# Kernel optimization log

Hardware: AMD Instinct MI355X
Metric: run time of the kernel (lower is better)

The kernel has to match this reference:

```python
import jax, jax.numpy as jnp
import numpy as np

B, N, C, H = 2, 2048, 1024, 16
D = C // H  # head_dim = 64


def setup_inputs() -> dict:
    key = jax.random.key(0)
    ks = jax.random.split(key, 10)
    s = 0.02
    return {
        "x": jax.random.normal(ks[0], (B, N, C), dtype=jnp.float32),
        "gauge_theta": jax.random.normal(ks[1], (C,), dtype=jnp.float32),
        "Wg": jax.random.normal(ks[2], (C, C), dtype=jnp.float32) * s,
        "bg": jnp.zeros((C,), dtype=jnp.float32),
        "Wqkv": jax.random.normal(ks[3], (3 * C, C), dtype=jnp.float32) * s,
        "bqkv": jnp.zeros((3 * C,), dtype=jnp.float32),
        "Wproj": jax.random.normal(ks[4], (C, C), dtype=jnp.float32) * s,
        "bproj": jnp.zeros((C,), dtype=jnp.float32),
    }


def reference(x, gauge_theta, Wg, bg, Wqkv, bqkv, Wproj, bproj):
    # gauge-equivariant mixing: x = x + 0.1 * (Linear(x) * theta)
    x_gauge = (jnp.einsum('bnc,oc->bno', x, Wg) + bg) * gauge_theta  # [B,N,C]
    xg = x + 0.1 * x_gauge
    # fused qkv projection -> [B,N,3,H,D] -> q,k,v [B,H,N,D]
    qkv = (jnp.einsum('bnc,oc->bno', xg, Wqkv) + bqkv).reshape(B, N, 3, H, D)
    qkv = jnp.transpose(qkv, (2, 0, 3, 1, 4))
    q, k, v = qkv[0], qkv[1], qkv[2]
    scale = 1.0 / jnp.sqrt(jnp.float32(D))
    attn = jnp.einsum('bhnd,bhmd->bhnm', q, k) * scale  # explicit [B,H,N,N]
    attn = jax.nn.softmax(attn, axis=-1)  # eval mode: no noise, no dropout
    out = jnp.einsum('bhnm,bhmd->bhnd', attn, v)  # [B,H,N,D]
    out = jnp.transpose(out, (0, 2, 1, 3)).reshape(B, N, C)
    return jnp.einsum('bnc,oc->bno', out, Wproj) + bproj
```

## Files before the change

### kernel.cpp

```cpp
#include <hip/hip_runtime.h>
#include <stdint.h>

typedef __bf16 bf16x8 __attribute__((ext_vector_type(8)));
typedef __bf16 bf16x2 __attribute__((ext_vector_type(2)));
typedef float  f32x4  __attribute__((ext_vector_type(4)));
typedef unsigned int u32x4 __attribute__((ext_vector_type(4)));
typedef unsigned short u16;

__device__ __forceinline__ u16 f2bf(float f) {
    return __builtin_bit_cast(u16, (__bf16)f);
}

__device__ __forceinline__ unsigned pk_bf16(float a, float b) {
    bf16x2 r; r[0] = (__bf16)a; r[1] = (__bf16)b;
    return __builtin_bit_cast(unsigned, r);
}

__device__ __forceinline__ bf16x8 ld_frag(const u16* p) {
    u32x4 u = *(const u32x4*)p;
    return __builtin_bit_cast(bf16x8, u);
}

__device__ __forceinline__ void gload16(const u16* g, u16* l) {
    __builtin_amdgcn_global_load_lds(
        (__attribute__((address_space(1))) void*)g,
        (__attribute__((address_space(3))) void*)l,
        16, 0, 0);
}

__device__ __forceinline__ int xcd_swz(int nwg) {
    int h = blockIdx.y * gridDim.x + blockIdx.x;
    return (h & 7) * (nwg >> 3) + (h >> 3);
}

#define ATT_CSC 0.18033688011112042f

__global__ __launch_bounds__(256) void cvt_all(
    const float* __restrict__ x, const float* __restrict__ wg,
    const float* __restrict__ wqkv, const float* __restrict__ wproj,
    u16* __restrict__ xo, u16* __restrict__ wgo,
    u16* __restrict__ wqkvo, u16* __restrict__ wprojo)
{
    int i = blockIdx.x * 256 + threadIdx.x;
    const float4* in; uint2* out; int off;
    if (i < 1048576)      { in = (const float4*)x;     out = (uint2*)xo;     off = i; }
    else if (i < 1310720) { in = (const float4*)wg;    out = (uint2*)wgo;    off = i - 1048576; }
    else if (i < 2097152) { in = (const float4*)wqkv;  out = (uint2*)wqkvo;  off = i - 1310720; }
    else                  { in = (const float4*)wproj; out = (uint2*)wprojo; off = i - 2097152; }
    float4 v = in[off];
    uint2 o; o.x = pk_bf16(v.x, v.y); o.y = pk_bf16(v.z, v.w);
    out[off] = o;
}

__global__ __launch_bounds__(512, 6) void gemm_bt(
    const u16* __restrict__ A,
    const u16* __restrict__ W,
    const float* __restrict__ bias,
    u16* __restrict__ qo, u16* __restrict__ ko, u16* __restrict__ vTo)
{
    __shared__ alignas(16) u16 As[128 * 64];
    __shared__ alignas(16) u16 Bs[128 * 64];
    const int tid  = threadIdx.x;
    const int wave = tid >> 6, lane = tid & 63;
    const int lquad = lane >> 4, lcol = lane & 15;
    const int wr = (wave >> 2) * 64, wc = (wave & 3) * 32;
    const int swzid = xcd_swz(768);
    const int rowb = (swzid & 31) * 128, colb = (swzid >> 5) * 128;
    const int srow8 = lane >> 3;
    const int swc = (((lane & 7) ^ srow8) * 8);
    const int rs0 = ((0 * 4 + lquad) ^ (lcol & 7)) * 8;
    const int rs1 = ((1 * 4 + lquad) ^ (lcol & 7)) * 8;

    const u16* gA = A + (size_t)(rowb + wave * 8 + srow8) * 1024 + swc;
    const u16* gB = W + (size_t)(colb + wave * 8 + srow8) * 1024 + swc;
    u16* dA = As + wave * 512;
    u16* dB = Bs + wave * 512;

    f32x4 zero4 = {0.f, 0.f, 0.f, 0.f};
    f32x4 acc[4][2];
#pragma unroll
    for (int i = 0; i < 4; i++)
#pragma unroll
        for (int j = 0; j < 2; j++) acc[i][j] = zero4;

    for (int k0 = 0; k0 < 1024; k0 += 64) {
        __syncthreads();
        gload16(gA + k0, dA);
        gload16(gA + (size_t)64 * 1024 + k0, dA + 64 * 64);
        gload16(gB + k0, dB);
        gload16(gB + (size_t)64 * 1024 + k0, dB + 64 * 64);
        __syncthreads();
#pragma unroll
        for (int db = 0; db < 2; db++) {
            const int rsw = db ? rs1 : rs0;
            bf16x8 af[4], bfr[2];
#pragma unroll
            for (int t = 0; t < 4; t++) af[t]  = ld_frag(As + (wr + t * 16 + lcol) * 64 + rsw);
#pragma unroll
            for (int t = 0; t < 2; t++) bfr[t] = ld_frag(Bs + (wc + t * 16 + lcol) * 64 + rsw);
#pragma unroll
            for (int i = 0; i < 4; i++)
#pragma unroll
                for (int j = 0; j < 2; j++)
                    acc[i][j] = __builtin_amdgcn_mfma_f32_16x16x32_bf16(af[i], bfr[j], acc[i][j], 0, 0, 0);
        }
    }

#pragma unroll
    for (int i = 0; i < 4; i++) {
#pragma unroll
        for (int j = 0; j < 2; j++) {
            int gcol = colb + wc + j * 16 + lcol;
            float bsv = bias[gcol];
            int grow0 = rowb + wr + i * 16 + lquad * 4;
            int three = gcol >> 10, rem = gcol & 1023;
            int h = rem >> 6, d = rem & 63;
            int b = grow0 >> 11, nn = grow0 & 2047;
            int bh = b * 16 + h;
            if (three == 2) {
                ushort4 o;
                o.x = f2bf(acc[i][j][0] + bsv);
                o.y = f2bf(acc[i][j][1] + bsv);
                o.z = f2bf(acc[i][j][2] + bsv);
                o.w = f2bf(acc[i][j][3] + bsv);
                *(ushort4*)(vTo + ((size_t)bh * 64 + d) * 2048 + nn) = o;
            } else if (three == 0) {
#pragma unroll
                for (int r = 0; r < 4; r++)
                    qo[((size_t)bh * 2048 + nn + r) * 64 + d] = f2bf((acc[i][j][r] + bsv) * ATT_CSC);
            } else {
#pragma unroll
                for (int r = 0; r < 4; r++)
                    ko[((size_t)bh * 2048 + nn + r) * 64 + d] = f2bf(acc[i][j][r] + bsv);
            }
        }
    }
}

__global__ __launch_bounds__(512, 4) void gemm64(
    int mode,
    const u16* __restrict__ A,
    const u16* __restrict__ W,
    const float* __restrict__ bias,
    const float* __restrict__ xres,
    const float* __restrict__ theta,
    u16* __restrict__ out_bf,
    float* __restrict__ out_f)
{
    __shared__ alignas(16) u16 As[64 * 64];
    __shared__ alignas(16) u16 Bs[128 * 64];
    const int tid  = threadIdx.x;
    const int wave = tid >> 6, lane = tid & 63;
    const int lquad = lane >> 4, lcol = lane & 15;
    const int wr = (wave & 1) * 32, wc = (wave >> 1) * 32;
    const int swzid = xcd_swz(512);
    const int rowb = (swzid & 63) * 64, colb = (swzid >> 6) * 128;
    const int srow8 = lane >> 3;
    const int swc = (((lane & 7) ^ srow8) * 8);
    const int rs0 = ((0 * 4 + lquad) ^ (lcol & 7)) * 8;
    const int rs1 = ((1 * 4 + lquad) ^ (lcol & 7)) * 8;

    const u16* gA = A + (size_t)(rowb + wave * 8 + srow8) * 1024 + swc;
    const u16* gB = W + (size_t)(colb + wave * 8 + srow8) * 1024 + swc;
    u16* dA = As + wave * 512;
    u16* dB = Bs + wave * 512;

    f32x4 zero4 = {0.f, 0.f, 0.f, 0.f};
    f32x4 acc[2][2];
#pragma unroll
    for (int i = 0; i < 2; i++)
#pragma unroll
        for (int j = 0; j < 2; j++) acc[i][j] = zero4;

    for (int k0 = 0; k0 < 1024; k0 += 64) {
        __syncthreads();
        gload16(gA + k0, dA);
        gload16(gB + k0, dB);
        gload16(gB + (size_t)64 * 1024 + k0, dB + 64 * 64);
        __syncthreads();
#pragma unroll
        for (int db = 0; db < 2; db++) {
            const int rsw = db ? rs1 : rs0;
            bf16x8 af[2], bfr[2];
#pragma unroll
            for (int t = 0; t < 2; t++) af[t]  = ld_frag(As + (wr + t * 16 + lcol) * 64 + rsw);
#pragma unroll
            for (int t = 0; t < 2; t++) bfr[t] = ld_frag(Bs + (wc + t * 16 + lcol) * 64 + rsw);
#pragma unroll
            for (int i = 0; i < 2; i++)
#pragma unroll
                for (int j = 0; j < 2; j++)
                    acc[i][j] = __builtin_amdgcn_mfma_f32_16x16x32_bf16(af[i], bfr[j], acc[i][j], 0, 0, 0);
        }
    }

#pragma unroll
    for (int i = 0; i < 2; i++) {
#pragma unroll
        for (int j = 0; j < 2; j++) {
            int gcol = colb + wc + j * 16 + lcol;
            float bsv = bias[gcol];
            int grow0 = rowb + wr + i * 16 + lquad * 4;
            if (mode == 0) {
#pragma unroll
                for (int r = 0; r < 4; r++) {
                    size_t idx = (size_t)(grow0 + r) * 1024 + gcol;
                    float val = acc[i][j][r] + bsv;
                    out_bf[idx] = f2bf(xres[idx] + 0.1f * (val * theta[gcol]));
                }
            } else {
#pragma unroll
                for (int r = 0; r < 4; r++)
                    out_f[(size_t)(grow0 + r) * 1024 + gcol] = acc[i][j][r] + bsv;
            }
        }
    }
}

__global__ __launch_bounds__(512, 4) void attn_kernel(
    const u16* __restrict__ q,
    const u16* __restrict__ k,
    const u16* __restrict__ vT,
    u16* __restrict__ attnout)
{
    __shared__ alignas(16) u16 smem[32768];

    const int tid  = threadIdx.x;
    const int wave = tid >> 6, lane = tid & 63;
    const int g = wave >> 2, wq = wave & 3;
    const int lquad = lane >> 4, lcol = lane & 15;
    const int swzid = xcd_swz(512);
    const int bh   = swzid >> 4;
    const int row0 = (swzid & 15) * 128 + wq * 32;
    const int rsw  = (lquad ^ (lcol & 3)) * 8;

    u16* KsG = smem + g * 8192;
    u16* VsG = smem + 16384 + g * 8192;

    bf16x8 qf[2][2];
#pragma unroll
    for (int qh = 0; qh < 2; qh++)
#pragma unroll
        for (int db = 0; db < 2; db++)
            qf[qh][db] = ld_frag(q + ((size_t)bh * 2048 + row0 + qh * 16 + lcol) * 64 + db * 32 + lquad * 8);

    const int sb = wq & 1;
    const int srow = lane >> 2;
    const int swc  = (((lane & 3) ^ (srow & 3)) * 8);
    const u16* gK = k  + ((size_t)bh * 2048 + srow) * 64 + sb * 32 + swc;
    const u16* gV = vT + ((size_t)bh * 64 + srow) * 2048 + sb * 32 + swc;

    auto stage = [&](int it, int buf) {
        int j0 = g * 1024 + it * 64;
        if ((wq & 2) == 0) {
            u16* ldst = KsG + buf * 4096 + sb * 2048;
#pragma unroll
            for (int i = 0; i < 4; i++)
                gload16(gK + (size_t)(j0 + i * 16) * 64, ldst + i * 16 * 32);
        } else {
            u16* ldst = VsG + buf * 4096 + sb * 2048;
#pragma unroll
            for (int i = 0; i < 4; i++)
                gload16(gV + (size_t)(i * 16) * 2048 + j0, ldst + i * 16 * 32);
        }
    };

    f32x4 zero4 = {0.f, 0.f, 0.f, 0.f};
    f32x4 lacc[2] = {zero4, zero4};
    f32x4 oacc[2][4];
#pragma unroll
    for (int qh = 0; qh < 2; qh++)
#pragma unroll
        for (int dt = 0; dt < 4; dt++) oacc[qh][dt] = zero4;

    stage(0, 0);
    __syncthreads();

    for (int it = 0; it < 16; ++it) {
        const int buf = it & 1;
        if (it < 15) stage(it + 1, buf ^ 1);

        const u16* Kt = KsG + buf * 4096;
        const u16* Vt = VsG + buf * 4096;

        f32x4 sacc[2][4];
        __builtin_amdgcn_s_setprio(1);
#pragma unroll
        for (int jt = 0; jt < 4; jt++)
#pragma unroll
            for (int db = 0; db < 2; db++) {
                bf16x8 kf = ld_frag(Kt + db * 2048 + (jt * 16 + lcol) * 32 + rsw);
#pragma unroll
                for (int qh = 0; qh < 2; qh++)
                    sacc[qh][jt] = __builtin_amdgcn_mfma_f32_16x16x32_bf16(
                        kf, qf[qh][db], db == 0 ? zero4 : sacc[qh][jt], 0, 0, 0);
            }
        __builtin_amdgcn_s_setprio(0);

        unsigned dpk[2][4][2];
#pragma unroll
        for (int qh = 0; qh < 2; qh++) {
#pragma unroll
            for (int jt = 0; jt < 4; jt++) {
                f32x4 pe;
                pe[0] = __builtin_amdgcn_exp2f(sacc[qh][jt][0]);
                pe[1] = __builtin_amdgcn_exp2f(sacc[qh][jt][1]);
                pe[2] = __builtin_amdgcn_exp2f(sacc[qh][jt][2]);
                pe[3] = __builtin_amdgcn_exp2f(sacc[qh][jt][3]);
                lacc[qh] += pe;
                dpk[qh][jt][0] = pk_bf16(pe[0], pe[1]);
                dpk[qh][jt][1] = pk_bf16(pe[2], pe[3]);
            }
        }

        bf16x8 pf[2][2];
#pragma unroll
        for (int qh = 0; qh < 2; qh++) {
#pragma unroll
            for (int kb = 0; kb < 2; kb++) {
                unsigned Ax = dpk[qh][2 * kb][0],     Ay = dpk[qh][2 * kb][1];
                unsigned Bx = dpk[qh][2 * kb + 1][0], By = dpk[qh][2 * kb + 1][1];
                u32x4 w;
#if __has_builtin(__builtin_amdgcn_permlane32_swap) && __has_builtin(__builtin_amdgcn_permlane16_swap)
                {
                    auto s1 = __builtin_amdgcn_permlane32_swap(Ax, Bx, false, false);
                    auto s2 = __builtin_amdgcn_permlane16_swap(s1[0], s1[1], false, false);
                    w[0] = s2[0]; w[2] = s2[1];
                    auto s3 = __builtin_amdgcn_permlane32_swap(Ay, By, false, false);
                    auto s4 = __builtin_amdgcn_permlane16_swap(s3[0], s3[1], false, false);
                    w[1] = s4[0]; w[3] = s4[1];
                }
#else
                {
                    unsigned x1x = (lquad < 2) ? Bx : Ax;
                    unsigned x1y = (lquad < 2) ? By : Ay;
                    unsigned r1x = __shfl_xor(x1x, 32, 64);
                    unsigned r1y = __shfl_xor(x1y, 32, 64);
                    unsigned x2x = (lquad == 1) ? Ax : (lquad == 2) ? Bx : r1x;
                    unsigned x2y = (lquad == 1) ? Ay : (lquad == 2) ? By : r1y;
                    unsigned r2x = __shfl_xor(x2x, 16, 64);
                    unsigned r2y = __shfl_xor(x2y, 16, 64);
                    w[0] = (lquad == 0) ? Ax : (lquad == 2) ? r1x : r2x;
                    w[1] = (lquad == 0) ? Ay : (lquad == 2) ? r1y : r2y;
                    w[2] = (lquad == 1) ? r1x : (lquad == 3) ? Bx : r2x;
                    w[3] = (lquad == 1) ? r1y : (lquad == 3) ? By : r2y;
                }
#endif
                pf[qh][kb] = __builtin_bit_cast(bf16x8, w);
            }
        }

        __builtin_amdgcn_s_setprio(1);
#pragma unroll
        for (int dt = 0; dt < 4; dt++)
#pragma unroll
            for (int kb = 0; kb < 2; kb++) {
                bf16x8 vf = ld_frag(Vt + kb * 2048 + (dt * 16 + lcol) * 32 + rsw);
#pragma unroll
                for (int qh = 0; qh < 2; qh++)
                    oacc[qh][dt] = __builtin_amdgcn_mfma_f32_16x16x32_bf16(vf, pf[qh][kb], oacc[qh][dt], 0, 0, 0);
            }
        __builtin_amdgcn_s_setprio(0);

        __syncthreads();
    }

    float* scr = (float*)smem;
    const int slot = wq * 64 + lane;
    if (g == 1) {
#pragma unroll
        for (int qh = 0; qh < 2; qh++) {
#pragma unroll
            for (int dt = 0; dt < 4; dt++)
                *(f32x4*)&scr[slot * 44 + qh * 16 + dt * 4] = oacc[qh][dt];
            *(f32x4*)&scr[slot * 44 + 32 + qh * 4] = lacc[qh];
        }
    }
    __syncthreads();
    if (g == 1) return;

#pragma unroll
    for (int qh = 0; qh < 2; qh++) {
#pragma unroll
        for (int dt = 0; dt < 4; dt++)
            oacc[qh][dt] += *(const f32x4*)&scr[slot * 44 + qh * 16 + dt * 4];
        lacc[qh] += *(const f32x4*)&scr[slot * 44 + 32 + qh * 4];
    }

    const int b = bh >> 4, h = bh & 15;
#pragma unroll
    for (int qh = 0; qh < 2; qh++) {
        float l = (lacc[qh][0] + lacc[qh][1]) + (lacc[qh][2] + lacc[qh][3]);
        l += __shfl_xor(l, 16, 64);
        l += __shfl_xor(l, 32, 64);
        float inv = 1.0f / l;
        const int n = row0 + qh * 16 + lcol;
        size_t base = ((size_t)b * 2048 + n) * 1024 + h * 64;
#pragma unroll
        for (int dt = 0; dt < 4; dt++) {
            uint2 o;
            o.x = pk_bf16(oacc[qh][dt][0] * inv, oacc[qh][dt][1] * inv);
            o.y = pk_bf16(oacc[qh][dt][2] * inv, oacc[qh][dt][3] * inv);
            *(uint2*)(attnout + base + dt * 16 + lquad * 4) = o;
        }
    }
}

extern "C" void kernel_launch(void* const* d_in, const int* in_sizes, int n_in,
                              void* d_out, int out_size, void* d_ws, size_t ws_size,
                              hipStream_t stream) {
    const float* x     = (const float*)d_in[0];
    const float* theta = (const float*)d_in[1];
    const float* Wg    = (const float*)d_in[2];
    const float* bg    = (const float*)d_in[3];
    const float* Wqkv  = (const float*)d_in[4];
    const float* bqkv  = (const float*)d_in[5];
    const float* Wproj = (const float*)d_in[6];
    const float* bproj = (const float*)d_in[7];
    float* out = (float*)d_out;

    unsigned char* ws = (unsigned char*)d_ws;
    const size_t MB = 1ull << 20;
    u16* x_bf     = (u16*)(ws + 0);
    u16* Wg_bf    = (u16*)(ws + 8 * MB);
    u16* Wqkv_bf  = (u16*)(ws + 10 * MB);
    u16* Wproj_bf = (u16*)(ws + 16 * MB);
    u16* xg_bf    = (u16*)(ws + 18 * MB);
    u16* q_bf     = (u16*)(ws + 26 * MB);
    u16* k_bf     = (u16*)(ws + 34 * MB);
    u16* vT_bf    = (u16*)(ws + 42 * MB);
    u16* ao_bf    = (u16*)(ws + 50 * MB);

    cvt_all<<<9216, 256, 0, stream>>>(x, Wg, Wqkv, Wproj,
                                      x_bf, Wg_bf, Wqkv_bf, Wproj_bf);

    gemm64<<<dim3(64, 8), dim3(512), 0, stream>>>(0, x_bf, Wg_bf, bg,
                                                  x, theta, xg_bf, nullptr);
    gemm_bt<<<dim3(32, 24), dim3(512), 0, stream>>>(xg_bf, Wqkv_bf, bqkv,
                                                    q_bf, k_bf, vT_bf);
    attn_kernel<<<dim3(16, 32), dim3(512), 0, stream>>>(q_bf, k_bf, vT_bf, ao_bf);
    gemm64<<<dim3(64, 8), dim3(512), 0, stream>>>(2, ao_bf, Wproj_bf, bproj,
                                                  nullptr, nullptr, nullptr, out);
}
```

Before: 202.9 us.

## Split attention KV range across four wave groups with 1024-thread blocks

The attention kernel now runs 1024 threads per block, with four groups of waves each covering a quarter of the key sequence instead of two groups covering halves. Each iteration stages 32 keys and uses a new K layout that keeps full 64-wide rows with an XOR swizzle. At the end, partial outputs are merged through shared memory in two passes. The aim is more parallelism and latency hiding per block, at the cost of more barriers in the merge, smaller per-iteration MFMA work, and register pressure from the launch bound of 8.

```diff
diff --git a/kernel.cpp b/kernel.cpp
--- a/kernel.cpp
+++ b/kernel.cpp
@@ -217,7 +217,7 @@
     }
 }
 
-__global__ __launch_bounds__(512, 4) void attn_kernel(
+__global__ __launch_bounds__(1024, 8) void attn_kernel(
     const u16* __restrict__ q,
     const u16* __restrict__ k,
     const u16* __restrict__ vT,
@@ -232,10 +232,8 @@
     const int swzid = xcd_swz(512);
     const int bh   = swzid >> 4;
     const int row0 = (swzid & 15) * 128 + wq * 32;
-    const int rsw  = (lquad ^ (lcol & 3)) * 8;
-
-    u16* KsG = smem + g * 8192;
-    u16* VsG = smem + 16384 + g * 8192;
+
+    u16* gbase = smem + g * 8192;
 
     bf16x8 qf[2][2];
 #pragma unroll
@@ -244,26 +242,32 @@
         for (int db = 0; db < 2; db++)
             qf[qh][db] = ld_frag(q + ((size_t)bh * 2048 + row0 + qh * 16 + lcol) * 64 + db * 32 + lquad * 8);
 
-    const int sb = wq & 1;
-    const int srow = lane >> 2;
-    const int swc  = (((lane & 3) ^ (srow & 3)) * 8);
-    const u16* gK = k  + ((size_t)bh * 2048 + srow) * 64 + sb * 32 + swc;
-    const u16* gV = vT + ((size_t)bh * 64 + srow) * 2048 + sb * 32 + swc;
+    const int krow = lane >> 3, kchk = lane & 7;
+    const int vrow = lane >> 2, vchk = lane & 3;
+    const u16* gK = k  + ((size_t)bh * 2048 + krow) * 64 + ((kchk ^ krow) * 8);
+    const u16* gV = vT + ((size_t)bh * 64 + vrow) * 2048 + ((vchk ^ (vrow & 3)) * 8);
+    const int roff = (wq & 1) * 16;
+    const int doff = (wq & 1) * 32;
 
     auto stage = [&](int it, int buf) {
-        int j0 = g * 1024 + it * 64;
+        int j0 = g * 512 + it * 32;
+        u16* base = gbase + buf * 4096;
         if ((wq & 2) == 0) {
-            u16* ldst = KsG + buf * 4096 + sb * 2048;
-#pragma unroll
-            for (int i = 0; i < 4; i++)
-                gload16(gK + (size_t)(j0 + i * 16) * 64, ldst + i * 16 * 32);
+#pragma unroll
+            for (int s = 0; s < 2; s++)
+                gload16(gK + (size_t)(j0 + roff + s * 8) * 64,
+                        base + (roff + s * 8) * 64);
         } else {
-            u16* ldst = VsG + buf * 4096 + sb * 2048;
-#pragma unroll
-            for (int i = 0; i < 4; i++)
-                gload16(gV + (size_t)(i * 16) * 2048 + j0, ldst + i * 16 * 32);
+#pragma unroll
+            for (int s = 0; s < 2; s++)
+                gload16(gV + (size_t)(doff + s * 16) * 2048 + j0,
+                        base + 2048 + (doff + s * 16) * 32);
         }
     };
+
+    const int rsK0 = ((0 * 4 + lquad) ^ (lcol & 7)) * 8;
+    const int rsK1 = ((1 * 4 + lquad) ^ (lcol & 7)) * 8;
+    const int rsV  = (lquad ^ (lcol & 3)) * 8;
 
     f32x4 zero4 = {0.f, 0.f, 0.f, 0.f};
     f32x4 lacc[2] = {zero4, zero4};
@@ -280,16 +284,16 @@
         const int buf = it & 1;
         if (it < 15) stage(it + 1, buf ^ 1);
 
-        const u16* Kt = KsG + buf * 4096;
-        const u16* Vt = VsG + buf * 4096;
-
-        f32x4 sacc[2][4];
+        const u16* Kt = gbase + buf * 4096;
+        const u16* Vt = Kt + 2048;
+
+        f32x4 sacc[2][2];
         __builtin_amdgcn_s_setprio(1);
 #pragma unroll
-        for (int jt = 0; jt < 4; jt++)
+        for (int jt = 0; jt < 2; jt++)
 #pragma unroll
             for (int db = 0; db < 2; db++) {
-                bf16x8 kf = ld_frag(Kt + db * 2048 + (jt * 16 + lcol) * 32 + rsw);
+                bf16x8 kf = ld_frag(Kt + (jt * 16 + lcol) * 64 + (db ? rsK1 : rsK0));
 #pragma unroll
                 for (int qh = 0; qh < 2; qh++)
                     sacc[qh][jt] = __builtin_amdgcn_mfma_f32_16x16x32_bf16(
@@ -297,11 +301,11 @@
             }
         __builtin_amdgcn_s_setprio(0);
 
-        unsigned dpk[2][4][2];
+        unsigned dpk[2][2][2];
 #pragma unroll
         for (int qh = 0; qh < 2; qh++) {
 #pragma unroll
-            for (int jt = 0; jt < 4; jt++) {
+            for (int jt = 0; jt < 2; jt++) {
                 f32x4 pe;
                 pe[0] = __builtin_amdgcn_exp2f(sacc[qh][jt][0]);
                 pe[1] = __builtin_amdgcn_exp2f(sacc[qh][jt][1]);
@@ -313,79 +317,78 @@
             }
         }
 
-        bf16x8 pf[2][2];
+        bf16x8 pf[2];
 #pragma unroll
         for (int qh = 0; qh < 2; qh++) {
-#pragma unroll
-            for (int kb = 0; kb < 2; kb++) {
-                unsigned Ax = dpk[qh][2 * kb][0],     Ay = dpk[qh][2 * kb][1];
-                unsigned Bx = dpk[qh][2 * kb + 1][0], By = dpk[qh][2 * kb + 1][1];
-                u32x4 w;
+            unsigned Ax = dpk[qh][0][0], Ay = dpk[qh][0][1];
+            unsigned Bx = dpk[qh][1][0], By = dpk[qh][1][1];
+            u32x4 w;
 #if __has_builtin(__builtin_amdgcn_permlane32_swap) && __has_builtin(__builtin_amdgcn_permlane16_swap)
-                {
-                    auto s1 = __builtin_amdgcn_permlane32_swap(Ax, Bx, false, false);
-                    auto s2 = __builtin_amdgcn_permlane16_swap(s1[0], s1[1], false, false);
-                    w[0] = s2[0]; w[2] = s2[1];
-                    auto s3 = __builtin_amdgcn_permlane32_swap(Ay, By, false, false);
-                    auto s4 = __builtin_amdgcn_permlane16_swap(s3[0], s3[1], false, false);
-                    w[1] = s4[0]; w[3] = s4[1];
-                }
+            {
+                auto s1 = __builtin_amdgcn_permlane32_swap(Ax, Bx, false, false);
+                auto s2 = __builtin_amdgcn_permlane16_swap(s1[0], s1[1], false, false);
+                w[0] = s2[0]; w[2] = s2[1];
+                auto s3 = __builtin_amdgcn_permlane32_swap(Ay, By, false, false);
+                auto s4 = __builtin_amdgcn_permlane16_swap(s3[0], s3[1], false, false);
+                w[1] = s4[0]; w[3] = s4[1];
+            }
 #else
-                {
-                    unsigned x1x = (lquad < 2) ? Bx : Ax;
-                    unsigned x1y = (lquad < 2) ? By : Ay;
-                    unsigned r1x = __shfl_xor(x1x, 32, 64);
-                    unsigned r1y = __shfl_xor(x1y, 32, 64);
-                    unsigned x2x = (lquad == 1) ? Ax : (lquad == 2) ? Bx : r1x;
-                    unsigned x2y = (lquad == 1) ? Ay : (lquad == 2) ? By : r1y;
-                    unsigned r2x = __shfl_xor(x2x, 16, 64);
-                    unsigned r2y = __shfl_xor(x2y, 16, 64);
-                    w[0] = (lquad == 0) ? Ax : (lquad == 2) ? r1x : r2x;
-                    w[1] = (lquad == 0) ? Ay : (lquad == 2) ? r1y : r2y;
-                    w[2] = (lquad == 1) ? r1x : (lquad == 3) ? Bx : r2x;
-                    w[3] = (lquad == 1) ? r1y : (lquad == 3) ? By : r2y;
-                }
+            {
+                unsigned x1x = (lquad < 2) ? Bx : Ax;
+                unsigned x1y = (lquad < 2) ? By : Ay;
+                unsigned r1x = __shfl_xor(x1x, 32, 64);
+                unsigned r1y = __shfl_xor(x1y, 32, 64);
+                unsigned x2x = (lquad == 1) ? Ax : (lquad == 2) ? Bx : r1x;
+                unsigned x2y = (lquad == 1) ? Ay : (lquad == 2) ? By : r1y;
+                unsigned r2x = __shfl_xor(x2x, 16, 64);
+                unsigned r2y = __shfl_xor(x2y, 16, 64);
+                w[0] = (lquad == 0) ? Ax : (lquad == 2) ? r1x : r2x;
+                w[1] = (lquad == 0) ? Ay : (lquad == 2) ? r1y : r2y;
+                w[2] = (lquad == 1) ? r1x : (lquad == 3) ? Bx : r2x;
+                w[3] = (lquad == 1) ? r1y : (lquad == 3) ? By : r2y;
+            }
 #endif
-                pf[qh][kb] = __builtin_bit_cast(bf16x8, w);
-            }
+            pf[qh] = __builtin_bit_cast(bf16x8, w);
         }
 
         __builtin_amdgcn_s_setprio(1);
 #pragma unroll
-        for (int dt = 0; dt < 4; dt++)
-#pragma unroll
-            for (int kb = 0; kb < 2; kb++) {
-                bf16x8 vf = ld_frag(Vt + kb * 2048 + (dt * 16 + lcol) * 32 + rsw);
-#pragma unroll
-                for (int qh = 0; qh < 2; qh++)
-                    oacc[qh][dt] = __builtin_amdgcn_mfma_f32_16x16x32_bf16(vf, pf[qh][kb], oacc[qh][dt], 0, 0, 0);
-            }
+        for (int dt = 0; dt < 4; dt++) {
+            bf16x8 vf = ld_frag(Vt + (dt * 16 + lcol) * 32 + rsV);
+#pragma unroll
+            for (int qh = 0; qh < 2; qh++)
+                oacc[qh][dt] = __builtin_amdgcn_mfma_f32_16x16x32_bf16(vf, pf[qh], oacc[qh][dt], 0, 0, 0);
+        }
         __builtin_amdgcn_s_setprio(0);
 
         __syncthreads();
     }
 
     float* scr = (float*)smem;
-    const int slot = wq * 64 + lane;
-    if (g == 1) {
-#pragma unroll
-        for (int qh = 0; qh < 2; qh++) {
+    const int tslot = wq * 64 + lane;
+#pragma unroll
+    for (int qh = 0; qh < 2; qh++) {
+        __syncthreads();
+        if (g != 0) {
+            int b0 = ((g - 1) * 256 + tslot) * 20;
 #pragma unroll
             for (int dt = 0; dt < 4; dt++)
-                *(f32x4*)&scr[slot * 44 + qh * 16 + dt * 4] = oacc[qh][dt];
-            *(f32x4*)&scr[slot * 44 + 32 + qh * 4] = lacc[qh];
-        }
-    }
-    __syncthreads();
-    if (g == 1) return;
-
-#pragma unroll
-    for (int qh = 0; qh < 2; qh++) {
-#pragma unroll
-        for (int dt = 0; dt < 4; dt++)
-            oacc[qh][dt] += *(const f32x4*)&scr[slot * 44 + qh * 16 + dt * 4];
-        lacc[qh] += *(const f32x4*)&scr[slot * 44 + 32 + qh * 4];
-    }
+                *(f32x4*)&scr[b0 + dt * 4] = oacc[qh][dt];
+            *(f32x4*)&scr[b0 + 16] = lacc[qh];
+        }
+        __syncthreads();
+        if (g == 0) {
+#pragma unroll
+            for (int gg = 0; gg < 3; gg++) {
+                int b0 = (gg * 256 + tslot) * 20;
+#pragma unroll
+                for (int dt = 0; dt < 4; dt++)
+                    oacc[qh][dt] += *(const f32x4*)&scr[b0 + dt * 4];
+                lacc[qh] += *(const f32x4*)&scr[b0 + 16];
+            }
+        }
+    }
+    if (g != 0) return;
 
     const int b = bh >> 4, h = bh & 15;
 #pragma unroll
@@ -438,7 +441,7 @@
                                                   x, theta, xg_bf, nullptr);
     gemm_bt<<<dim3(32, 24), dim3(512), 0, stream>>>(xg_bf, Wqkv_bf, bqkv,
                                                     q_bf, k_bf, vT_bf);
-    attn_kernel<<<dim3(16, 32), dim3(512), 0, stream>>>(q_bf, k_bf, vT_bf, ao_bf);
+    attn_kernel<<<dim3(16, 32), dim3(1024), 0, stream>>>(q_bf, k_bf, vT_bf, ao_bf);
     gemm64<<<dim3(64, 8), dim3(512), 0, stream>>>(2, ao_bf, Wproj_bf, bproj,
                                                   nullptr, nullptr, nullptr, out);
 }
```

Result: slower. 528.3 us (+160.4%).
